# Kernel optimization log

Hardware: AMD Instinct MI355X
Metric: run time of the kernel (lower is better)

## Reference

```python
import jax, jax.numpy as jnp
import numpy as np

N_NODES = 100000
N_EDGES = 1600000
NFEAT, NHID0, NHID1, NCLASS = 256, 128, 128, 40


def setup_inputs() -> dict:
    key = jax.random.key(0)
    ks = jax.random.split(key, 8)
    x = jax.random.normal(ks[0], (N_NODES, NFEAT), dtype=jnp.float32)
    edge_index = jax.random.randint(ks[1], (2, N_EDGES), 0, N_NODES, dtype=jnp.int32)
    # Glorot-ish scaled weights for the 3 GCNConv layers (nhid=2 hidden + output)
    W0 = jax.random.normal(ks[2], (NFEAT, NHID0), dtype=jnp.float32) / np.sqrt(NFEAT)
    b0 = jnp.zeros((NHID0,), dtype=jnp.float32)
    W1 = jax.random.normal(ks[3], (NHID0, NHID1), dtype=jnp.float32) / np.sqrt(NHID0)
    b1 = jnp.zeros((NHID1,), dtype=jnp.float32)
    W2 = jax.random.normal(ks[4], (NHID1, NCLASS), dtype=jnp.float32) / np.sqrt(NHID1)
    b2 = jnp.zeros((NCLASS,), dtype=jnp.float32)
    return {"x": x, "edge_index": edge_index, "W0": W0, "b0": b0,
            "W1": W1, "b1": b1, "W2": W2, "b2": b2}


def reference(x, edge_index, W0, b0, W1, b1, W2, b2):
    N = x.shape[0]
    self_loop = jnp.arange(N, dtype=edge_index.dtype)
    src = jnp.concatenate([edge_index[0], self_loop])  # message sources j
    dst = jnp.concatenate([edge_index[1], self_loop])  # message targets i
    # Symmetric GCN normalization with self-loops: D^{-1/2} (A+I) D^{-1/2}
    deg = jax.ops.segment_sum(jnp.ones_like(src, dtype=x.dtype), dst, num_segments=N)
    dinv = jnp.where(deg > 0, jax.lax.rsqrt(jnp.maximum(deg, 1.0)), 0.0)
    norm = (dinv[src] * dinv[dst])[:, None]  # [E+N, 1]

    def gcn_conv(h, W, b):
        m = h @ W                              # transform first (PyG GCNConv)
        agg = jax.ops.segment_sum(m[src] * norm, dst, num_segments=N)
        return agg + b

    # forward applies ReLU (and dropout, a no-op in eval) after EVERY layer incl. last
    h = jax.nn.relu(gcn_conv(x, W0, b0))
    h = jax.nn.relu(gcn_conv(h, W1, b1))
    h = jax.nn.relu(gcn_conv(h, W2, b2))
    return jax.nn.log_softmax(h, axis=1)
```

## Files before the change

kernel.cpp:

```cpp
#include <hip/hip_runtime.h>
#include <hip/hip_bf16.h>
#include <hip/hip_fp16.h>
#include <math.h>

#define NHID 128
#define NCLASS 40
#define NBLK 256
#define MAXBUK 1600

typedef _Float16 f16;
typedef f16 f16x8 __attribute__((ext_vector_type(8)));
typedef float f32x4 __attribute__((ext_vector_type(4)));


__global__ __launch_bounds__(256) void bucket_hist(const int* __restrict__ dst,
                                                   int* __restrict__ bh,
                                                   int E, int nbuk, int chunk) {
    __shared__ int h[MAXBUK];
    for (int i = threadIdx.x; i < nbuk; i += 256) h[i] = 0;
    __syncthreads();
    int b = blockIdx.x;
    int lo = b * chunk, hi = min(E, lo + chunk);
    for (int e = lo + threadIdx.x; e < hi; e += 256) atomicAdd(&h[dst[e] >> 6], 1);
    __syncthreads();
    for (int i = threadIdx.x; i < nbuk; i += 256) bh[(size_t)b * nbuk + i] = h[i];
}

__global__ __launch_bounds__(256) void bucket_total(const int* __restrict__ bh,
                                                    int* __restrict__ T, int nbuk) {
    int buk = blockIdx.x * 256 + threadIdx.x;
    if (buk >= nbuk) return;
    int s = 0;
    for (int b = 0; b < NBLK; ++b) s += bh[(size_t)b * nbuk + buk];
    T[buk] = s;
}

__global__ __launch_bounds__(256) void bucket_scan(const int* __restrict__ T,
                                                   int* __restrict__ BB, int nbuk, int E) {
    __shared__ int sc[256];
    __shared__ int carry;
    if (threadIdx.x == 0) carry = 0;
    __syncthreads();
    for (int base = 0; base < nbuk; base += 256) {
        int i = base + threadIdx.x;
        int v = (i < nbuk) ? T[i] : 0;
        sc[threadIdx.x] = v;
        __syncthreads();
        for (int off = 1; off < 256; off <<= 1) {
            int t = (threadIdx.x >= off) ? sc[threadIdx.x - off] : 0;
            __syncthreads();
            sc[threadIdx.x] += t;
            __syncthreads();
        }
        if (i < nbuk) BB[i] = carry + sc[threadIdx.x] - v;
        __syncthreads();
        if (threadIdx.x == 255) carry += sc[255];
        __syncthreads();
    }
    if (threadIdx.x == 0) BB[nbuk] = E;
}

__global__ __launch_bounds__(256) void bucket_expand(const int* __restrict__ bh,
                                                     const int* __restrict__ BB,
                                                     int* __restrict__ off, int nbuk) {
    int buk = blockIdx.x * 256 + threadIdx.x;
    if (buk >= nbuk) return;
    int run = BB[buk];
    for (int b = 0; b < NBLK; ++b) {
        off[(size_t)b * nbuk + buk] = run;
        run += bh[(size_t)b * nbuk + buk];
    }
}

__global__ __launch_bounds__(256) void bucket_scatter(const int* __restrict__ src,
                                                      const int* __restrict__ dst,
                                                      const int* __restrict__ off,
                                                      int2* __restrict__ eb,
                                                      int E, int nbuk, int chunk) {
    __shared__ int cur[MAXBUK];
    int b = blockIdx.x;
    for (int i = threadIdx.x; i < nbuk; i += 256) cur[i] = off[(size_t)b * nbuk + i];
    __syncthreads();
    int lo = b * chunk, hi = min(E, lo + chunk);
    for (int e = lo + threadIdx.x; e < hi; e += 256) {
        int d = dst[e], s = src[e];
        int pos = atomicAdd(&cur[d >> 6], 1);
        eb[pos] = make_int2(s, d);
    }
}

__global__ __launch_bounds__(256) void bucket_csr(const int2* __restrict__ eb,
                                                  const int* __restrict__ BB,
                                                  int* __restrict__ startA,
                                                  float* __restrict__ dinv,
                                                  int* __restrict__ col,
                                                  int N, int E) {
    __shared__ int h[64];
    int b = blockIdx.x;
    int bs = BB[b], be = BB[b + 1];
    if (threadIdx.x < 64) h[threadIdx.x] = 0;
    __syncthreads();
    for (int i = bs + threadIdx.x; i < be; i += 256) atomicAdd(&h[eb[i].y & 63], 1);
    __syncthreads();
    if (threadIdx.x < 64) {
        int v = h[threadIdx.x];
        int incl = v;
#pragma unroll
        for (int o = 1; o < 64; o <<= 1) {
            int t = __shfl_up(incl, o, 64);
            if ((int)threadIdx.x >= o) incl += t;
        }
        int n = (b << 6) + threadIdx.x;
        if (n < N) {
            startA[n] = bs + incl - v;
            dinv[n] = rsqrtf((float)(v + 1));
        }
        h[threadIdx.x] = incl - v;
    }
    __syncthreads();
    for (int i = bs + threadIdx.x; i < be; i += 256) {
        int2 p = eb[i];
        int pos = bs + atomicAdd(&h[p.y & 63], 1);
        col[pos] = p.x;
    }
    if (b == 0 && threadIdx.x == 0) startA[N] = E;
}

template <int K, int BM, int BN, int WM, int WN, bool GUARDN, bool AHALF>
__global__ __launch_bounds__(256) void gemm_mfma(const void* __restrict__ Ap,
                                                 const float* __restrict__ W,
                                                 const float* __restrict__ dinv,
                                                 f16* __restrict__ C, int M, int N) {
    constexpr int KC = 64;
    __shared__ f16 As[BM * KC];
    __shared__ f16 Bs[BN * KC];
    __shared__ float sdinv[BM];
    const int t = threadIdx.x;
    const int wid = t >> 6, lane = t & 63;
    const int wm = wid % WM, wn = wid / WM;
    const int row0 = blockIdx.x * BM;

    for (int i = t; i < BM; i += 256) {
        int r = row0 + i;
        sdinv[i] = dinv[r < M ? r : M - 1];
    }

    f32x4 acc[4][4] = {};

    for (int k0 = 0; k0 < K; k0 += KC) {
        if (AHALF) {
            const f16* A = (const f16*)Ap;
#pragma unroll
            for (int i = 0; i < BM / 32; ++i) {
                int g = t + i * 256;
                int r = g >> 3, c = g & 7;
                int grow = row0 + r; if (grow >= M) grow = M - 1;
                f16x8 v = *reinterpret_cast<const f16x8*>(&A[(size_t)grow * K + k0 + c * 8]);
                *reinterpret_cast<f16x8*>(&As[r * 64 + ((c ^ (r & 7)) << 3)]) = v;
            }
        } else {
            const float* A = (const float*)Ap;
#pragma unroll
            for (int i = 0; i < BM / 32; ++i) {
                int g = t + i * 256;
                int r = g >> 3, c = g & 7;
                int grow = row0 + r; if (grow >= M) grow = M - 1;
                const float* s = &A[(size_t)grow * K + k0 + c * 8];
                float4 a = *reinterpret_cast<const float4*>(s);
                float4 b = *reinterpret_cast<const float4*>(s + 4);
                f16x8 v = {(f16)a.x, (f16)a.y, (f16)a.z, (f16)a.w,
                           (f16)b.x, (f16)b.y, (f16)b.z, (f16)b.w};
                *reinterpret_cast<f16x8*>(&As[r * 64 + ((c ^ (r & 7)) << 3)]) = v;
            }
        }
        if (!GUARDN) {
#pragma unroll
            for (int i = 0; i < BN / 16; ++i) {
                int v = t + i * 256;
                int kk = v / (BN / 4), nq = v % (BN / 4);
                float4 w = *reinterpret_cast<const float4*>(&W[(size_t)(k0 + kk) * N + nq * 4]);
                float ws[4] = {w.x, w.y, w.z, w.w};
#pragma unroll
                for (int j = 0; j < 4; ++j) {
                    int n = nq * 4 + j;
                    Bs[n * 64 + (((kk >> 3) ^ (n & 7)) << 3) + (kk & 7)] = (f16)ws[j];
                }
            }
        } else {
#pragma unroll
            for (int i = 0; i < BN / 16; ++i) {
                int v = t + i * 256;
                int kk = v / (BN / 4), nq = v % (BN / 4);
#pragma unroll
                for (int j = 0; j < 4; ++j) {
                    int n = nq * 4 + j;
                    float wv = (n < N) ? W[(size_t)(k0 + kk) * N + n] : 0.f;
                    Bs[n * 64 + (((kk >> 3) ^ (n & 7)) << 3) + (kk & 7)] = (f16)wv;
                }
            }
        }
        __syncthreads();

#pragma unroll
        for (int s = 0; s < 2; ++s) {
            f16x8 af[4], bf[4];
            int c = s * 4 + (lane >> 4);
#pragma unroll
            for (int mf = 0; mf < 4; ++mf) {
                int r = wm * 64 + mf * 16 + (lane & 15);
                af[mf] = *reinterpret_cast<const f16x8*>(&As[r * 64 + ((c ^ (r & 7)) << 3)]);
            }
#pragma unroll
            for (int nf = 0; nf < 4; ++nf) {
                int n = wn * 64 + nf * 16 + (lane & 15);
                bf[nf] = *reinterpret_cast<const f16x8*>(&Bs[n * 64 + ((c ^ (n & 7)) << 3)]);
            }
#pragma unroll
            for (int mf = 0; mf < 4; ++mf)
#pragma unroll
                for (int nf = 0; nf < 4; ++nf)
                    acc[mf][nf] = __builtin_amdgcn_mfma_f32_16x16x32_f16(af[mf], bf[nf],
                                                                         acc[mf][nf], 0, 0, 0);
        }
        __syncthreads();
    }

#pragma unroll
    for (int mf = 0; mf < 4; ++mf) {
#pragma unroll
        for (int q = 0; q < 4; ++q) {
            int lr = wm * 64 + mf * 16 + (lane >> 4) * 4 + q;
            int grow = row0 + lr;
            if (grow < M) {
                float scl = sdinv[lr];
#pragma unroll
                for (int nf = 0; nf < 4; ++nf) {
                    int gcol = wn * 64 + nf * 16 + (lane & 15);
                    if (!GUARDN || gcol < N)
                        C[(size_t)grow * N + gcol] = (f16)(acc[mf][nf][q] * scl);
                }
            }
        }
    }
}

__global__ __launch_bounds__(256) void agg_h_kernel(
        const __half* __restrict__ m, const int* __restrict__ col,
        const int* __restrict__ start,
        const float* __restrict__ dinv, const float* __restrict__ bias,
        __half* __restrict__ out, int N) {
    int w = (int)((blockIdx.x * 256 + threadIdx.x) >> 6);
    int lane = threadIdx.x & 63;
    if (w >= N) return;
    const __half2* mp = reinterpret_cast<const __half2*>(m);
    int s = start[w];
    int e = start[w + 1];
    float ax = 0.f, ay = 0.f, bx = 0.f, by = 0.f;
    int p = s;
    for (; p + 8 <= e; p += 8) {
        int j[8];
#pragma unroll
        for (int u = 0; u < 8; ++u) j[u] = col[p + u];
        __half2 v[8];
#pragma unroll
        for (int u = 0; u < 8; ++u) v[u] = mp[j[u] * 64 + lane];
#pragma unroll
        for (int u = 0; u < 8; ++u) {
            float2 f = __half22float2(v[u]);
            if (u & 1) { bx += f.x; by += f.y; }
            else       { ax += f.x; ay += f.y; }
        }
    }
    for (; p < e; ++p) {
        float2 f = __half22float2(mp[col[p] * 64 + lane]);
        ax += f.x; ay += f.y;
    }
    float2 fi = __half22float2(mp[w * 64 + lane]);
    ax += fi.x; ay += fi.y;
    float di = dinv[w];
    float ox = fmaxf(fmaf(di, ax + bx, bias[lane * 2]), 0.f);
    float oy = fmaxf(fmaf(di, ay + by, bias[lane * 2 + 1]), 0.f);
    reinterpret_cast<__half2*>(out)[w * 64 + lane] = __floats2half2_rn(ox, oy);
}

__global__ __launch_bounds__(256) void agg_out_kernel(
        const __half* __restrict__ m, const int* __restrict__ col,
        const int* __restrict__ start,
        const float* __restrict__ dinv, const float* __restrict__ bias,
        float* __restrict__ out, int N) {
    int w = (int)((blockIdx.x * 256 + threadIdx.x) >> 6);
    int lane = threadIdx.x & 63;
    if (w >= N) return;
    bool act = lane < NCLASS;
    int cl = act ? lane : 0;
    int s = start[w];
    int e = start[w + 1];
    float a0 = 0.f, a1 = 0.f;
    int p = s;
    for (; p + 8 <= e; p += 8) {
        int j[8];
#pragma unroll
        for (int u = 0; u < 8; ++u) j[u] = col[p + u];
        __half v[8];
#pragma unroll
        for (int u = 0; u < 8; ++u) v[u] = m[j[u] * NCLASS + cl];
#pragma unroll
        for (int u = 0; u < 8; ++u) {
            if (u & 1) a1 += __half2float(v[u]);
            else       a0 += __half2float(v[u]);
        }
    }
    for (; p < e; ++p) a0 += __half2float(m[col[p] * NCLASS + cl]);
    a0 += __half2float(m[w * NCLASS + cl]);
    float di = dinv[w];
    float h = fmaxf(fmaf(di, a0 + a1, bias[cl]), 0.f);
    float hm = act ? h : -INFINITY;
#pragma unroll
    for (int off = 32; off; off >>= 1) hm = fmaxf(hm, __shfl_xor(hm, off, 64));
    float ex = act ? expf(h - hm) : 0.f;
    float se = ex;
#pragma unroll
    for (int off = 32; off; off >>= 1) se += __shfl_xor(se, off, 64);
    if (act) out[(size_t)w * NCLASS + lane] = h - hm - logf(se);
}


extern "C" void kernel_launch(void* const* d_in, const int* in_sizes, int n_in,
                              void* d_out, int out_size, void* d_ws, size_t ws_size,
                              hipStream_t stream) {
    const float* x  = (const float*)d_in[0];
    const int*   ei = (const int*)d_in[1];
    const float* W0 = (const float*)d_in[2];
    const float* b0 = (const float*)d_in[3];
    const float* W1 = (const float*)d_in[4];
    const float* b1 = (const float*)d_in[5];
    const float* W2 = (const float*)d_in[6];
    const float* b2 = (const float*)d_in[7];
    float* out = (float*)d_out;

    const int NFEATr = 256;
    const int N = in_sizes[0] / NFEATr;
    const int E = in_sizes[1] / 2;
    const int* src = ei;
    const int* dst = ei + E;

    const int nbuk = (N + 63) >> 6;
    const int chunk = (E + NBLK - 1) / NBLK;

    char* p = (char*)d_ws;
    auto alloc = [&](size_t bytes) -> void* {
        void* r = (void*)p;
        p += (bytes + 255) & ~(size_t)255;
        return r;
    };
    int*    bh     = (int*)alloc((size_t)NBLK * nbuk * 4);
    int*    T      = (int*)alloc((size_t)nbuk * 4);
    int*    BB     = (int*)alloc((size_t)(nbuk + 1) * 4);
    int*    offb   = (int*)alloc((size_t)NBLK * nbuk * 4);
    int2*   eb     = (int2*)alloc((size_t)E * 8);
    int*    col    = (int*)alloc((size_t)E * 4);
    int*    startA = (int*)alloc((size_t)(N + 1) * 4);
    float*  dinv   = (float*)alloc((size_t)N * 4);
    f16*    mbuf   = (f16*)alloc((size_t)N * NHID * 2);
    f16*    hbuf   = (f16*)alloc((size_t)N * NHID * 2);

    int nbl7 = (nbuk + 255) / 256;

    bucket_hist<<<NBLK, 256, 0, stream>>>(dst, bh, E, nbuk, chunk);
    bucket_total<<<nbl7, 256, 0, stream>>>(bh, T, nbuk);
    bucket_scan<<<1, 256, 0, stream>>>(T, BB, nbuk, E);
    bucket_expand<<<nbl7, 256, 0, stream>>>(bh, BB, offb, nbuk);
    bucket_scatter<<<NBLK, 256, 0, stream>>>(src, dst, offb, eb, E, nbuk, chunk);
    bucket_csr<<<nbuk, 256, 0, stream>>>(eb, BB, startA, dinv, col, N, E);

    int abl = (N + 3) / 4;
    int g128 = (N + 127) / 128;
    int g256 = (N + 255) / 256;

    gemm_mfma<256, 128, 128, 2, 2, false, false><<<g128, 256, 0, stream>>>(
        (const void*)x, W0, dinv, mbuf, N, NHID);
    agg_h_kernel<<<abl, 256, 0, stream>>>((const __half*)mbuf, col, startA, dinv, b0,
                                          (__half*)hbuf, N);

    gemm_mfma<128, 128, 128, 2, 2, false, true><<<g128, 256, 0, stream>>>(
        (const void*)hbuf, W1, dinv, mbuf, N, NHID);
    agg_h_kernel<<<abl, 256, 0, stream>>>((const __half*)mbuf, col, startA, dinv, b1,
                                          (__half*)hbuf, N);

    gemm_mfma<128, 256, 64, 4, 1, true, true><<<g256, 256, 0, stream>>>(
        (const void*)hbuf, W2, dinv, mbuf, N, NCLASS);
    agg_out_kernel<<<abl, 256, 0, stream>>>((const __half*)mbuf, col, startA, dinv, b2,
                                            out, N);
}
```

Baseline: 378.3 us.

## Gather four edges per wavefront with 16-byte loads and pack bucket edges

The aggregation kernels now split each 64-lane wavefront into four groups of 16 lanes. Each group handles a different neighbor edge and loads 8 fp16 features at once (4 in the output layer), and the partial sums are combined with cross-lane shuffles. This replaces the old scheme where every lane loaded one half2 per edge. Separately, the bucket scatter packs src and the low six bits of dst into a single int, which halves the temporary edge buffer traffic. The packing assumes src fits in 25 bits, and the new aggregation adds shuffle reductions and idle lanes on partial edge groups.

Result: no change. 383.4 us (+1.3%).

```diff
diff --git a/kernel.cpp b/kernel.cpp
--- a/kernel.cpp
+++ b/kernel.cpp
@@ -10,6 +10,7 @@
 
 typedef _Float16 f16;
 typedef f16 f16x8 __attribute__((ext_vector_type(8)));
+typedef f16 f16x4 __attribute__((ext_vector_type(4)));
 typedef float f32x4 __attribute__((ext_vector_type(4)));
 
 
@@ -75,7 +76,7 @@
 __global__ __launch_bounds__(256) void bucket_scatter(const int* __restrict__ src,
                                                       const int* __restrict__ dst,
                                                       const int* __restrict__ off,
-                                                      int2* __restrict__ eb,
+                                                      int* __restrict__ eb,
                                                       int E, int nbuk, int chunk) {
     __shared__ int cur[MAXBUK];
     int b = blockIdx.x;
@@ -85,11 +86,11 @@
     for (int e = lo + threadIdx.x; e < hi; e += 256) {
         int d = dst[e], s = src[e];
         int pos = atomicAdd(&cur[d >> 6], 1);
-        eb[pos] = make_int2(s, d);
-    }
-}
-
-__global__ __launch_bounds__(256) void bucket_csr(const int2* __restrict__ eb,
+        eb[pos] = (s << 6) | (d & 63);
+    }
+}
+
+__global__ __launch_bounds__(256) void bucket_csr(const int* __restrict__ eb,
                                                   const int* __restrict__ BB,
                                                   int* __restrict__ startA,
                                                   float* __restrict__ dinv,
@@ -100,7 +101,7 @@
     int bs = BB[b], be = BB[b + 1];
     if (threadIdx.x < 64) h[threadIdx.x] = 0;
     __syncthreads();
-    for (int i = bs + threadIdx.x; i < be; i += 256) atomicAdd(&h[eb[i].y & 63], 1);
+    for (int i = bs + threadIdx.x; i < be; i += 256) atomicAdd(&h[eb[i] & 63], 1);
     __syncthreads();
     if (threadIdx.x < 64) {
         int v = h[threadIdx.x];
@@ -119,9 +120,9 @@
     }
     __syncthreads();
     for (int i = bs + threadIdx.x; i < be; i += 256) {
-        int2 p = eb[i];
-        int pos = bs + atomicAdd(&h[p.y & 63], 1);
-        col[pos] = p.x;
+        int pk = eb[i];
+        int pos = bs + atomicAdd(&h[pk & 63], 1);
+        col[pos] = pk >> 6;
     }
     if (b == 0 && threadIdx.x == 0) startA[N] = E;
 }
@@ -245,83 +246,116 @@
 }
 
 __global__ __launch_bounds__(256) void agg_h_kernel(
-        const __half* __restrict__ m, const int* __restrict__ col,
-        const int* __restrict__ start,
-        const float* __restrict__ dinv, const float* __restrict__ bias,
-        __half* __restrict__ out, int N) {
+        const f16* __restrict__ m, const int* __restrict__ col,
+        const int* __restrict__ start, const float* __restrict__ dinv,
+        const float* __restrict__ bias, f16* __restrict__ out, int N) {
     int w = (int)((blockIdx.x * 256 + threadIdx.x) >> 6);
     int lane = threadIdx.x & 63;
     if (w >= N) return;
-    const __half2* mp = reinterpret_cast<const __half2*>(m);
-    int s = start[w];
-    int e = start[w + 1];
-    float ax = 0.f, ay = 0.f, bx = 0.f, by = 0.f;
-    int p = s;
-    for (; p + 8 <= e; p += 8) {
-        int j[8];
-#pragma unroll
-        for (int u = 0; u < 8; ++u) j[u] = col[p + u];
-        __half2 v[8];
-#pragma unroll
-        for (int u = 0; u < 8; ++u) v[u] = mp[j[u] * 64 + lane];
-#pragma unroll
-        for (int u = 0; u < 8; ++u) {
-            float2 f = __half22float2(v[u]);
-            if (u & 1) { bx += f.x; by += f.y; }
-            else       { ax += f.x; ay += f.y; }
-        }
-    }
-    for (; p < e; ++p) {
-        float2 f = __half22float2(mp[col[p] * 64 + lane]);
-        ax += f.x; ay += f.y;
-    }
-    float2 fi = __half22float2(mp[w * 64 + lane]);
-    ax += fi.x; ay += fi.y;
-    float di = dinv[w];
-    float ox = fmaxf(fmaf(di, ax + bx, bias[lane * 2]), 0.f);
-    float oy = fmaxf(fmaf(di, ay + by, bias[lane * 2 + 1]), 0.f);
-    reinterpret_cast<__half2*>(out)[w * 64 + lane] = __floats2half2_rn(ox, oy);
+    const int eg = lane >> 4, fl = lane & 15;
+    int s = start[w], e = start[w + 1];
+    float a[8] = {};
+    int full = s + ((e - s) & ~3);
+    for (int p = s; p < full; p += 4) {
+        int j = col[p + eg];
+        f16x8 v = *reinterpret_cast<const f16x8*>(&m[(size_t)j * 128 + fl * 8]);
+#pragma unroll
+        for (int u = 0; u < 8; ++u) a[u] += (float)v[u];
+    }
+    if (full < e) {
+        int idx = full + eg;
+        bool val = idx < e;
+        int j = col[val ? idx : s];
+        f16x8 v = *reinterpret_cast<const f16x8*>(&m[(size_t)j * 128 + fl * 8]);
+        if (val) {
+#pragma unroll
+            for (int u = 0; u < 8; ++u) a[u] += (float)v[u];
+        }
+    }
+    if (eg == 0) {
+        f16x8 v = *reinterpret_cast<const f16x8*>(&m[(size_t)w * 128 + fl * 8]);
+#pragma unroll
+        for (int u = 0; u < 8; ++u) a[u] += (float)v[u];
+    }
+#pragma unroll
+    for (int off = 16; off <= 32; off <<= 1)
+#pragma unroll
+        for (int u = 0; u < 8; ++u) a[u] += __shfl_xor(a[u], off, 64);
+    if (eg == 0) {
+        float di = dinv[w];
+        float4 bA = *reinterpret_cast<const float4*>(&bias[fl * 8]);
+        float4 bB = *reinterpret_cast<const float4*>(&bias[fl * 8 + 4]);
+        float bb[8] = {bA.x, bA.y, bA.z, bA.w, bB.x, bB.y, bB.z, bB.w};
+        f16x8 o;
+#pragma unroll
+        for (int u = 0; u < 8; ++u) o[u] = (f16)fmaxf(fmaf(di, a[u], bb[u]), 0.f);
+        *reinterpret_cast<f16x8*>(&out[(size_t)w * 128 + fl * 8]) = o;
+    }
 }
 
 __global__ __launch_bounds__(256) void agg_out_kernel(
-        const __half* __restrict__ m, const int* __restrict__ col,
-        const int* __restrict__ start,
-        const float* __restrict__ dinv, const float* __restrict__ bias,
-        float* __restrict__ out, int N) {
+        const f16* __restrict__ m, const int* __restrict__ col,
+        const int* __restrict__ start, const float* __restrict__ dinv,
+        const float* __restrict__ bias, float* __restrict__ out, int N) {
     int w = (int)((blockIdx.x * 256 + threadIdx.x) >> 6);
     int lane = threadIdx.x & 63;
     if (w >= N) return;
-    bool act = lane < NCLASS;
-    int cl = act ? lane : 0;
-    int s = start[w];
-    int e = start[w + 1];
-    float a0 = 0.f, a1 = 0.f;
-    int p = s;
-    for (; p + 8 <= e; p += 8) {
-        int j[8];
-#pragma unroll
-        for (int u = 0; u < 8; ++u) j[u] = col[p + u];
-        __half v[8];
-#pragma unroll
-        for (int u = 0; u < 8; ++u) v[u] = m[j[u] * NCLASS + cl];
-#pragma unroll
-        for (int u = 0; u < 8; ++u) {
-            if (u & 1) a1 += __half2float(v[u]);
-            else       a0 += __half2float(v[u]);
-        }
-    }
-    for (; p < e; ++p) a0 += __half2float(m[col[p] * NCLASS + cl]);
-    a0 += __half2float(m[w * NCLASS + cl]);
+    const int eg = lane >> 4, fl = lane & 15;
+    const bool act = fl < 10;
+    const int base = fl * 4;
+    int s = start[w], e = start[w + 1];
+    float a[4] = {};
+    int full = s + ((e - s) & ~3);
+    for (int p = s; p < full; p += 4) {
+        int j = col[p + eg];
+        if (act) {
+            f16x4 v = *reinterpret_cast<const f16x4*>(&m[(size_t)j * NCLASS + base]);
+#pragma unroll
+            for (int u = 0; u < 4; ++u) a[u] += (float)v[u];
+        }
+    }
+    if (full < e) {
+        int idx = full + eg;
+        bool val = idx < e;
+        int j = col[val ? idx : s];
+        if (act) {
+            f16x4 v = *reinterpret_cast<const f16x4*>(&m[(size_t)j * NCLASS + base]);
+            if (val) {
+#pragma unroll
+                for (int u = 0; u < 4; ++u) a[u] += (float)v[u];
+            }
+        }
+    }
+    if (eg == 0 && act) {
+        f16x4 v = *reinterpret_cast<const f16x4*>(&m[(size_t)w * NCLASS + base]);
+#pragma unroll
+        for (int u = 0; u < 4; ++u) a[u] += (float)v[u];
+    }
+#pragma unroll
+    for (int off = 16; off <= 32; off <<= 1)
+#pragma unroll
+        for (int u = 0; u < 4; ++u) a[u] += __shfl_xor(a[u], off, 64);
     float di = dinv[w];
-    float h = fmaxf(fmaf(di, a0 + a1, bias[cl]), 0.f);
-    float hm = act ? h : -INFINITY;
-#pragma unroll
-    for (int off = 32; off; off >>= 1) hm = fmaxf(hm, __shfl_xor(hm, off, 64));
-    float ex = act ? expf(h - hm) : 0.f;
-    float se = ex;
-#pragma unroll
-    for (int off = 32; off; off >>= 1) se += __shfl_xor(se, off, 64);
-    if (act) out[(size_t)w * NCLASS + lane] = h - hm - logf(se);
+    float h[4];
+    float mx = -INFINITY;
+#pragma unroll
+    for (int u = 0; u < 4; ++u) {
+        h[u] = act ? fmaxf(fmaf(di, a[u], bias[base + u]), 0.f) : -INFINITY;
+        mx = fmaxf(mx, h[u]);
+    }
+#pragma unroll
+    for (int off = 1; off <= 8; off <<= 1) mx = fmaxf(mx, __shfl_xor(mx, off, 64));
+    float se = 0.f;
+#pragma unroll
+    for (int u = 0; u < 4; ++u) se += act ? expf(h[u] - mx) : 0.f;
+#pragma unroll
+    for (int off = 1; off <= 8; off <<= 1) se += __shfl_xor(se, off, 64);
+    if (eg == 0 && act) {
+        float ls = logf(se);
+        float4 o = make_float4(h[0] - mx - ls, h[1] - mx - ls,
+                               h[2] - mx - ls, h[3] - mx - ls);
+        *reinterpret_cast<float4*>(&out[(size_t)w * NCLASS + base]) = o;
+    }
 }
 
 
@@ -357,7 +391,7 @@
     int*    T      = (int*)alloc((size_t)nbuk * 4);
     int*    BB     = (int*)alloc((size_t)(nbuk + 1) * 4);
     int*    offb   = (int*)alloc((size_t)NBLK * nbuk * 4);
-    int2*   eb     = (int2*)alloc((size_t)E * 8);
+    int*    eb     = (int*)alloc((size_t)E * 4);
     int*    col    = (int*)alloc((size_t)E * 4);
     int*    startA = (int*)alloc((size_t)(N + 1) * 4);
     float*  dinv   = (float*)alloc((size_t)N * 4);
@@ -379,16 +413,13 @@
 
     gemm_mfma<256, 128, 128, 2, 2, false, false><<<g128, 256, 0, stream>>>(
         (const void*)x, W0, dinv, mbuf, N, NHID);
-    agg_h_kernel<<<abl, 256, 0, stream>>>((const __half*)mbuf, col, startA, dinv, b0,
-                                          (__half*)hbuf, N);
+    agg_h_kernel<<<abl, 256, 0, stream>>>(mbuf, col, startA, dinv, b0, hbuf, N);
 
     gemm_mfma<128, 128, 128, 2, 2, false, true><<<g128, 256, 0, stream>>>(
         (const void*)hbuf, W1, dinv, mbuf, N, NHID);
-    agg_h_kernel<<<abl, 256, 0, stream>>>((const __half*)mbuf, col, startA, dinv, b1,
-                                          (__half*)hbuf, N);
+    agg_h_kernel<<<abl, 256, 0, stream>>>(mbuf, col, startA, dinv, b1, hbuf, N);
 
     gemm_mfma<128, 256, 64, 4, 1, true, true><<<g256, 256, 0, stream>>>(
         (const void*)hbuf, W2, dinv, mbuf, N, NCLASS);
-    agg_out_kernel<<<abl, 256, 0, stream>>>((const __half*)mbuf, col, startA, dinv, b2,
-                                            out, N);
-}
+    agg_out_kernel<<<abl, 256, 0, stream>>>(mbuf, col, startA, dinv, b2, out, N);
+}
```
